# Kernel tuning notes

Measured on AMD Instinct MI355X. Metric: run time of the kernel, lower is better.

Reference implementation:

```python
import jax, jax.numpy as jnp
import numpy as np

B, N, D = 4, 2048, 256
EPS = 1e-5


def _clinear(Z, W, b):
    # complex linear: Z (B,2,N,din), W (2,dout,din), b (2,dout)
    Zr, Zi = Z[:, 0], Z[:, 1]
    Wr, Wi = W[0], W[1]
    outr = Zr @ Wr.T - Zi @ Wi.T + b[0]
    outi = Zr @ Wi.T + Zi @ Wr.T + b[1]
    return jnp.stack([outr, outi], axis=1)


def setup_inputs() -> dict:
    key = jax.random.key(0)
    ks = jax.random.split(key, 14)
    sc = 1.0 / np.sqrt(D).astype(np.float32)
    t = jnp.tile(jnp.arange(N + 1, dtype=jnp.float32)[None] * 0.01, (B, 1))
    return {
        'Z_q': jax.random.normal(ks[0], (B, 2, N, D), jnp.float32),
        'Z_k': jax.random.normal(ks[1], (B, 2, N, D), jnp.float32),
        'Z_v': jax.random.normal(ks[2], (B, 2, N, D), jnp.float32),
        't_measure_all': t,
        'W_q': jax.random.normal(ks[3], (2, D, D), jnp.float32) * sc,
        'b_q': jax.random.normal(ks[4], (2, D), jnp.float32) * 0.01,
        'W_k': jax.random.normal(ks[5], (2, D, D), jnp.float32) * sc,
        'b_k': jax.random.normal(ks[6], (2, D), jnp.float32) * 0.01,
        'W_v': jax.random.normal(ks[7], (2, D, D), jnp.float32) * sc,
        'b_v': jax.random.normal(ks[8], (2, D), jnp.float32) * 0.01,
        'W_p': jax.random.normal(ks[9], (2, D, D), jnp.float32) * sc,
        'b_p': jax.random.normal(ks[10], (2, D), jnp.float32) * 0.01,
        'lambda1': jax.random.normal(ks[11], (2, D // 2, 1), jnp.float32),
        'lambda_Omega_sqrt': jax.random.normal(ks[12], (1, D, 1), jnp.float32) * sc,
        'lambda_Gamma_sqrt': jax.random.normal(ks[13], (1, D, 1), jnp.float32) * sc,
        'tau': jnp.asarray(1.0, jnp.float32),
        'delta': jnp.asarray(0.0, jnp.float32),
        'lambda_C': jnp.ones((1, D, 1), jnp.float32),
    }


def reference(Z_q, Z_k, Z_v, t_measure_all, W_q, b_q, W_k, b_k, W_v, b_v,
              W_p, b_p, lambda1, lambda_Omega_sqrt, lambda_Gamma_sqrt,
              tau, delta, lambda_C):
    # lambda_h = 0 * compute_lambda_h(lambda1): conjugate-pair spectrum, zeroed in forward
    lam_r = 0.0 * jnp.concatenate([lambda1[0], lambda1[0]], axis=0)[:, 0]   # (D,)
    lam_i = 0.0 * jnp.concatenate([lambda1[1], -lambda1[1]], axis=0)[:, 0]  # (D,)
    lam_Om = lambda_Omega_sqrt ** 2 + EPS   # process noise (1,D,1)
    lam_Ga = lambda_Gamma_sqrt ** 2 + EPS   # measurement noise (1,D,1)

    Q = _clinear(Z_q, W_q, b_q)  # (B,2,N,D)
    K = _clinear(Z_k, W_k, b_k)
    V = _clinear(Z_v, W_v, b_v)

    t = t_measure_all[0, :-1]  # (N,)
    # exponential state-transition kernels exp(+/- lambda * t): (2,N,D)
    mag_f = jnp.exp(lam_r[None] * t[:, None]); ph_f = lam_i[None] * t[:, None]
    exp_f = jnp.stack([mag_f * jnp.cos(ph_f), mag_f * jnp.sin(ph_f)])
    mag_b = jnp.exp(-lam_r[None] * t[:, None]); ph_b = -lam_i[None] * t[:, None]
    exp_b = jnp.stack([mag_b * jnp.cos(ph_b), mag_b * jnp.sin(ph_b)])
    # one-step transition exp(lambda * dt): (2,D)
    dt = t[1] - t[0]
    mat_exp = jnp.stack([jnp.exp(lam_r * dt) * jnp.cos(lam_i * dt),
                         jnp.exp(lam_r * dt) * jnp.sin(lam_i * dt)])

    # averaged covariance kernel, exact lambda->0 limit: Gamma + Omega*|t_i-t_j|, mean over D
    lamC2 = lambda_C[0, :, 0] ** 2
    ga_bar = jnp.mean(lamC2 * lam_Ga[0, :, 0])
    om_bar = jnp.mean(lamC2 * lam_Om[0, :, 0])
    abs_dt = jnp.abs(t[:, None] - t[None, :])          # (N,N)
    V_avg_ij = ga_bar + om_bar * abs_dt                # (N,N)

    # factorized kernels
    V_v = exp_f[None]                 # (1,2,N,D)
    U_q = exp_b[None] * Q             # (B,2,N,D)
    U_k = exp_b[None] * K
    U_v = exp_b[None] * V

    # precision-weighted squared residual norm R_ij = sum_d |V_k|^2 |U_q_i - U_k_j|^2
    Vk_abs = jnp.sum(exp_f ** 2, axis=0)              # (N,D)
    Uk_abs = jnp.sum(U_k ** 2, axis=1)                # (B,N,D)
    Uq_abs = jnp.sum(U_q ** 2, axis=1)                # (B,N,D)
    T1 = jnp.einsum('id,bjd->bij', Vk_abs, Uk_abs)
    T2 = jnp.sum(Vk_abs[None] * Uq_abs, axis=2)[:, :, None]
    T3 = (jnp.einsum('bid,bjd->bij', Vk_abs[None] * U_q[:, 0], U_k[:, 0]) +
          jnp.einsum('bid,bjd->bij', Vk_abs[None] * U_q[:, 1], U_k[:, 1]))
    R_qk_abs = T1 + T2 - 2.0 * T3                     # (B,N,N)

    scores = -(tau ** 2) * jnp.log(V_avg_ij[None] + R_qk_abs)
    mask = jnp.tril(jnp.ones((N, N), bool))
    scores = jnp.where(mask[None], scores, -jnp.inf)
    A = jax.nn.softmax(scores, axis=2)                # (B,N,N)
    Q_ij = jnp.stack([A, jnp.zeros_like(A)], axis=1)  # (B,2,N,N)

    # est_inner = complex matmul(Q_ij, U_v); Q imag part is zero
    est_inner = jnp.stack([jnp.einsum('bij,bjd->bid', A, U_v[:, 0]),
                           jnp.einsum('bij,bjd->bid', A, U_v[:, 1])], axis=1)
    est_v = V_v * est_inner          # plain elementwise product, as in source
    s = jax.nn.sigmoid(delta)
    est_eigenbasis = (1.0 - s) * V + s * est_v        # (B,2,N,D)

    # complex Hadamard with one-step transition
    pr = mat_exp[0][None, None] * est_eigenbasis[:, 0] - mat_exp[1][None, None] * est_eigenbasis[:, 1]
    pi = mat_exp[0][None, None] * est_eigenbasis[:, 1] + mat_exp[1][None, None] * est_eigenbasis[:, 0]
    pred_p = jnp.stack([pr, pi], axis=1)
    out = _clinear(pred_p, W_p, b_p)                  # (B,2,N,D)

    lambda_h = jnp.stack([lam_r, lam_i])[..., None]
    return est_eigenbasis, out, Q_ij, V_v, U_v, lambda_h
```

## Files before the change

### kernel.cpp

```cpp
#include <hip/hip_runtime.h>
#include <math.h>

#define BN 4
#define NN 2048
#define DD 256
#define EPSF 1e-5f

typedef __attribute__((ext_vector_type(8))) short bf16x8;
typedef __attribute__((ext_vector_type(4))) float f32x4;

constexpr size_t OFF_EST = 0;
constexpr size_t OFF_OUT = (size_t)BN * 2 * NN * DD;
constexpr size_t OFF_QIJ = OFF_OUT + (size_t)BN * 2 * NN * DD;
constexpr size_t OFF_VV  = OFF_QIJ + (size_t)BN * 2 * NN * NN;
constexpr size_t OFF_UV  = OFF_VV + (size_t)2 * NN * DD;
constexpr size_t OFF_LH  = OFF_UV + (size_t)BN * 2 * NN * DD;

constexpr size_t SCR_B0   = OFF_QIJ + (size_t)NN * NN;
constexpr size_t U_Q16    = 0;
constexpr size_t U_K16    = (size_t)BN * NN * DD;
constexpr size_t U_VT16   = 2 * (size_t)BN * NN * DD;
constexpr size_t SCR_QN   = SCR_B0 + 3 * (size_t)BN * NN * DD / 2;
constexpr size_t SCR_KN   = SCR_QN + (size_t)BN * NN;
constexpr size_t SCR_L    = SCR_KN + (size_t)BN * NN;
constexpr size_t SCR_SC   = SCR_L + (size_t)BN * NN;
constexpr size_t SCR_E16F = OFF_QIJ + 3 * (size_t)NN * NN;
constexpr size_t SCR_Z16F = OFF_QIJ + 5 * (size_t)NN * NN;
constexpr size_t SCR_Z16VF = OFF_QIJ + 7 * (size_t)NN * NN;
constexpr size_t U_W16    = (size_t)BN * NN * 512;

__device__ __forceinline__ short f2bf(float x) {
    union { float f; unsigned u; } v; v.f = x;
    unsigned r = v.u + 0x7fff + ((v.u >> 16) & 1);
    return (short)(r >> 16);
}
__device__ __forceinline__ float bf2f(unsigned short h) {
    union { unsigned u; float f; } v; v.u = ((unsigned)h) << 16;
    return v.f;
}
__device__ __forceinline__ unsigned short* u16p(float* d, size_t fofs) {
    return (unsigned short*)(d + fofs);
}
__device__ __forceinline__ const unsigned short* u16pc(const float* d, size_t fofs) {
    return (const unsigned short*)(d + fofs);
}

__global__ void k_prep(const float* __restrict__ tau, const float* __restrict__ delta,
                       const float* __restrict__ lamOm, const float* __restrict__ lamGa,
                       const float* __restrict__ lamC, float* __restrict__ dout) {
    __shared__ float red[8];
    const int t = threadIdx.x;
    float c2 = lamC[t] * lamC[t];
    float ga = c2 * (lamGa[t] * lamGa[t] + EPSF);
    float om = c2 * (lamOm[t] * lamOm[t] + EPSF);
    for (int o = 32; o > 0; o >>= 1) {
        ga += __shfl_down(ga, o, 64);
        om += __shfl_down(om, o, 64);
    }
    if ((t & 63) == 0) { red[t >> 6] = ga; red[4 + (t >> 6)] = om; }
    __syncthreads();
    if (t == 0) {
        float gs = red[0] + red[1] + red[2] + red[3];
        float os = red[4] + red[5] + red[6] + red[7];
        float* scal = dout + SCR_SC;
        scal[0] = tau[0] * tau[0];
        scal[1] = 1.f / (1.f + __expf(-delta[0]));
        scal[2] = gs / 256.f;
        scal[3] = os / 256.f;
    }
    float* Z = dout + SCR_QN;
    for (int i = t; i < 3 * BN * NN; i += 256) Z[i] = 0.f;
}

__global__ void k_zero_est(float* __restrict__ dout) {
    const int b = blockIdx.y;
    float* p = dout + OFF_EST + (size_t)(2 * b) * NN * DD;
    const size_t i = ((size_t)blockIdx.x * 256 + threadIdx.x) * 4;
    *(float4*)&p[i] = (float4){0.f, 0.f, 0.f, 0.f};
}

__global__ void k_cvt(const float* __restrict__ Zq, const float* __restrict__ Zk,
                      const float* __restrict__ Zv,
                      const float* __restrict__ Wq, const float* __restrict__ Wk,
                      const float* __restrict__ Wv, const float* __restrict__ Wp,
                      float* __restrict__ dout) {
    const int z = blockIdx.z;
    if (z < 3) {
        const float* Z = (z == 0) ? Zq : (z == 1) ? Zk : Zv;
        unsigned short* O = (z == 0) ? u16p(dout, SCR_Z16F)
                          : (z == 1) ? u16p(dout, SCR_Z16F) + (size_t)BN * NN * 512
                                     : u16p(dout, SCR_Z16VF);
        const long n4 = (long)BN * 2 * NN * DD / 4;
        for (long i4 = (long)blockIdx.x * 256 + threadIdx.x; i4 < n4;
             i4 += (long)gridDim.x * 256) {
            const long i = i4 * 4;
            const int d = (int)(i & (DD - 1));
            const long r = i >> 8;
            const int n = (int)(r & (NN - 1));
            const long bc = r >> 11;
            const int c = (int)(bc & 1), b = (int)(bc >> 1);
            float4 v = *(const float4*)&Z[i];
            ushort4 o;
            o.x = (unsigned short)f2bf(v.x); o.y = (unsigned short)f2bf(v.y);
            o.z = (unsigned short)f2bf(v.z); o.w = (unsigned short)f2bf(v.w);
            *(ushort4*)&O[((size_t)(b * NN + n)) * 512 + c * 256 + d] = o;
        }
    } else {
        const float* Ws[4] = {Wq, Wk, Wv, Wp};
        unsigned short* W16 = u16p(dout, SCR_Z16VF) + U_W16;
        const long n4 = 6L * 256 * 512 / 4;
        for (long e4 = (long)blockIdx.x * 256 + threadIdx.x; e4 < n4;
             e4 += (long)gridDim.x * 256) {
            const long e = e4 * 4;
            const int k = (int)(e & 511);
            const long rest = e >> 9;
            const int dd = (int)(rest & 255);
            const int m = (int)(rest >> 8);
            int proj, mode;
            if (m < 3)      { proj = m; mode = 0; }
            else if (m == 3){ proj = 2; mode = 1; }
            else            { proj = 3; mode = m - 4; }
            const int kc = k >> 8, kk = k & 255;
            int wc; float sgn;
            if (mode == 0) { wc = kc; sgn = kc ? -1.f : 1.f; }
            else           { wc = 1 - kc; sgn = 1.f; }
            float4 v = *(const float4*)&Ws[proj][((size_t)wc * DD + dd) * DD + kk];
            ushort4 o;
            o.x = (unsigned short)f2bf(sgn * v.x); o.y = (unsigned short)f2bf(sgn * v.y);
            o.z = (unsigned short)f2bf(sgn * v.z); o.w = (unsigned short)f2bf(sgn * v.w);
            *(ushort4*)&W16[(size_t)m * 256 * 512 + (size_t)dd * 512 + k] = o;
        }
    }
}

__global__ __launch_bounds__(256) void k_qkv(const float* __restrict__ bq,
                                             const float* __restrict__ bk,
                                             const float* __restrict__ bv,
                                             float* __restrict__ dout)
{
    __shared__ short Al[128 * 40];
    __shared__ short Bl[128 * 40];
    const int z = blockIdx.z;
    const int d0 = blockIdx.x * 128;
    const int b = blockIdx.y >> 4;
    const int n0 = (blockIdx.y & 15) * 128;

    const unsigned short* Z16 =
        (z == 0) ? u16pc(dout, SCR_Z16F)
      : (z == 1) ? u16pc(dout, SCR_Z16F) + (size_t)BN * NN * 512
                 : u16pc(dout, SCR_Z16VF);
    const unsigned short* W16 = u16pc(dout, SCR_Z16VF) + U_W16 + (size_t)z * 256 * 512;
    const float* bias = (z == 0) ? bq : (z == 1) ? bk : bv;
    const int bofs = (z == 3) ? DD : 0;

    const int t = threadIdx.x, wave = t >> 6, lane = t & 63, quad = lane >> 4, lm = lane & 15;
    const int wm = (wave >> 1) * 64, wn = (wave & 1) * 64;
    const int srow = t >> 1, sch = (t & 1) * 16;

    f32x4 acc[4][4];
#pragma unroll
    for (int i = 0; i < 4; ++i)
#pragma unroll
        for (int j = 0; j < 4; ++j) acc[i][j] = (f32x4){0.f, 0.f, 0.f, 0.f};

    for (int kt = 0; kt < 16; ++kt) {
        const int kk0 = kt * 32;
        const unsigned short* Za = Z16 + ((size_t)(b * NN + n0 + srow)) * 512 + kk0 + sch;
        bf16x8 a0 = *(const bf16x8*)(Za + 0);
        bf16x8 a1 = *(const bf16x8*)(Za + 8);
        const unsigned short* Wa = W16 + (size_t)(d0 + srow) * 512 + kk0 + sch;
        bf16x8 w0 = *(const bf16x8*)(Wa + 0);
        bf16x8 w1 = *(const bf16x8*)(Wa + 8);
        __syncthreads();
        *(bf16x8*)&Al[srow * 40 + sch]     = a0;
        *(bf16x8*)&Al[srow * 40 + sch + 8] = a1;
        *(bf16x8*)&Bl[srow * 40 + sch]     = w0;
        *(bf16x8*)&Bl[srow * 40 + sch + 8] = w1;
        __syncthreads();
        bf16x8 af[4], bff[4];
#pragma unroll
        for (int mi = 0; mi < 4; ++mi) af[mi] = *(const bf16x8*)&Al[(wm + mi * 16 + lm) * 40 + quad * 8];
#pragma unroll
        for (int nj = 0; nj < 4; ++nj) bff[nj] = *(const bf16x8*)&Bl[(wn + nj * 16 + lm) * 40 + quad * 8];
#pragma unroll
        for (int mi = 0; mi < 4; ++mi)
#pragma unroll
            for (int nj = 0; nj < 4; ++nj)
                acc[mi][nj] = __builtin_amdgcn_mfma_f32_16x16x32_bf16(af[mi], bff[nj], acc[mi][nj], 0, 0, 0);
    }

    if (z <= 1) {
        unsigned short* O16 = u16p(dout, SCR_B0) + (z ? U_K16 : U_Q16) + (size_t)b * NN * DD;
        float* NRM = dout + (z ? SCR_KN : SCR_QN) + b * NN;
#pragma unroll
        for (int mi = 0; mi < 4; ++mi)
#pragma unroll
            for (int r = 0; r < 4; ++r) {
                const int m = n0 + wm + mi * 16 + quad * 4 + r;
                float ss = 0.f;
#pragma unroll
                for (int nj = 0; nj < 4; ++nj) {
                    const int d = d0 + wn + nj * 16 + lm;
                    unsigned short h = (unsigned short)f2bf(acc[mi][nj][r] + bias[d]);
                    O16[(size_t)m * DD + d] = h;
                    const float vb = bf2f(h);
                    ss = fmaf(vb, vb, ss);
                }
                ss += __shfl_down(ss, 8, 16); ss += __shfl_down(ss, 4, 16);
                ss += __shfl_down(ss, 2, 16); ss += __shfl_down(ss, 1, 16);
                if (lm == 0) atomicAdd(&NRM[m], ss);
            }
    } else if (z == 2) {
        float* UV0 = dout + OFF_UV + (size_t)(b * 2) * NN * DD;
#pragma unroll
        for (int mi = 0; mi < 4; ++mi)
#pragma unroll
            for (int r = 0; r < 4; ++r) {
                const int m = n0 + wm + mi * 16 + quad * 4 + r;
#pragma unroll
                for (int nj = 0; nj < 4; ++nj) {
                    const int d = d0 + wn + nj * 16 + lm;
                    UV0[(size_t)m * DD + d] = acc[mi][nj][r] + bias[d];
                }
            }
    } else {
        const float s1 = 1.f - dout[SCR_SC + 1];
        float* EST1 = dout + OFF_EST + (size_t)(b * 2 + 1) * NN * DD;
        unsigned short* E16 = u16p(dout, SCR_E16F) + (size_t)b * NN * 512;
#pragma unroll
        for (int mi = 0; mi < 4; ++mi)
#pragma unroll
            for (int r = 0; r < 4; ++r) {
                const int m = n0 + wm + mi * 16 + quad * 4 + r;
#pragma unroll
                for (int nj = 0; nj < 4; ++nj) {
                    const int d = d0 + wn + nj * 16 + lm;
                    const float v = s1 * (acc[mi][nj][r] + bias[bofs + d]);
                    EST1[(size_t)m * DD + d] = v;
                    E16[(size_t)m * 512 + 256 + d] = (unsigned short)f2bf(v);
                }
            }
    }
}

__global__ __launch_bounds__(256) void k_outproj(const float* __restrict__ bp,
                                                 float* __restrict__ dout)
{
    __shared__ short Al[128 * 40];
    __shared__ short Bl[128 * 40];
    const int z = blockIdx.z;
    const int d0 = blockIdx.x * 128;
    const int b = blockIdx.y >> 4;
    const int n0 = (blockIdx.y & 15) * 128;
    const unsigned short* E16 = u16pc(dout, SCR_E16F) + (size_t)b * NN * 512;
    const unsigned short* W16 = u16pc(dout, SCR_Z16VF) + U_W16 + (size_t)(4 + z) * 256 * 512;

    const int t = threadIdx.x, wave = t >> 6, lane = t & 63, quad = lane >> 4, lm = lane & 15;
    const int wm = (wave >> 1) * 64, wn = (wave & 1) * 64;
    const int srow = t >> 1, sch = (t & 1) * 16;

    f32x4 acc[4][4];
#pragma unroll
    for (int i = 0; i < 4; ++i)
#pragma unroll
        for (int j = 0; j < 4; ++j) acc[i][j] = (f32x4){0.f, 0.f, 0.f, 0.f};

    for (int kt = 0; kt < 16; ++kt) {
        const int kk0 = kt * 32;
        const unsigned short* Za = E16 + ((size_t)(n0 + srow)) * 512 + kk0 + sch;
        bf16x8 a0 = *(const bf16x8*)(Za + 0);
        bf16x8 a1 = *(const bf16x8*)(Za + 8);
        const unsigned short* Wa = W16 + (size_t)(d0 + srow) * 512 + kk0 + sch;
        bf16x8 w0 = *(const bf16x8*)(Wa + 0);
        bf16x8 w1 = *(const bf16x8*)(Wa + 8);
        __syncthreads();
        *(bf16x8*)&Al[srow * 40 + sch]     = a0;
        *(bf16x8*)&Al[srow * 40 + sch + 8] = a1;
        *(bf16x8*)&Bl[srow * 40 + sch]     = w0;
        *(bf16x8*)&Bl[srow * 40 + sch + 8] = w1;
        __syncthreads();
        bf16x8 af[4], bff[4];
#pragma unroll
        for (int mi = 0; mi < 4; ++mi) af[mi] = *(const bf16x8*)&Al[(wm + mi * 16 + lm) * 40 + quad * 8];
#pragma unroll
        for (int nj = 0; nj < 4; ++nj) bff[nj] = *(const bf16x8*)&Bl[(wn + nj * 16 + lm) * 40 + quad * 8];
#pragma unroll
        for (int mi = 0; mi < 4; ++mi)
#pragma unroll
            for (int nj = 0; nj < 4; ++nj)
                acc[mi][nj] = __builtin_amdgcn_mfma_f32_16x16x32_bf16(af[mi], bff[nj], acc[mi][nj], 0, 0, 0);
    }
    const int bofs = z ? DD : 0;
    float* O = dout + OFF_OUT + (size_t)(b * 2 + z) * NN * DD;
#pragma unroll
    for (int mi = 0; mi < 4; ++mi)
#pragma unroll
        for (int r = 0; r < 4; ++r) {
            const int m = n0 + wm + mi * 16 + quad * 4 + r;
#pragma unroll
            for (int nj = 0; nj < 4; ++nj) {
                const int d = d0 + wn + nj * 16 + lm;
                O[(size_t)m * DD + d] = acc[mi][nj][r] + bp[bofs + d];
            }
        }
}

__global__ void k_vtrans(float* __restrict__ dout) {
    __shared__ float T[64][65];
    const int b = blockIdx.z;
    const int nb = blockIdx.x * 64, db = blockIdx.y * 64;
    const float* V = dout + OFF_UV + (size_t)(b * 2) * NN * DD;
    unsigned short* VT = u16p(dout, SCR_B0) + U_VT16 + (size_t)b * DD * NN;
    const int tr = threadIdx.x >> 4, tc = (threadIdx.x & 15) * 4;
#pragma unroll
    for (int p = 0; p < 4; ++p) {
        float4 v = *(const float4*)&V[(size_t)(nb + tr + p * 16) * DD + db + tc];
        T[tr + p * 16][tc + 0] = v.x; T[tr + p * 16][tc + 1] = v.y;
        T[tr + p * 16][tc + 2] = v.z; T[tr + p * 16][tc + 3] = v.w;
    }
    __syncthreads();
#pragma unroll
    for (int p = 0; p < 4; ++p) {
        const int d = tr + p * 16;
        ushort4 o;
        o.x = (unsigned short)f2bf(T[tc + 0][d]);
        o.y = (unsigned short)f2bf(T[tc + 1][d]);
        o.z = (unsigned short)f2bf(T[tc + 2][d]);
        o.w = (unsigned short)f2bf(T[tc + 3][d]);
        *(ushort4*)&VT[(size_t)(db + d) * NN + nb + tc] = o;
    }
}

__global__ __launch_bounds__(256) void k_scores(const float* __restrict__ tmeas,
                                                float* __restrict__ dout) {
    __shared__ short Al[128 * 40];
    __shared__ short Bl[128 * 40];
    const int b = blockIdx.y, x = blockIdx.x;
    int ti = (int)((sqrtf(8.f * x + 1.f) - 1.f) * 0.5f);
    while ((ti + 1) * (ti + 2) / 2 <= x) ++ti;
    while (ti * (ti + 1) / 2 > x) --ti;
    const int tj = x - ti * (ti + 1) / 2;
    const int i0 = ti * 128, j0 = tj * 128;
    const unsigned short* Q16 = u16pc(dout, SCR_B0) + U_Q16 + (size_t)b * NN * DD;
    const unsigned short* K16 = u16pc(dout, SCR_B0) + U_K16 + (size_t)b * NN * DD;
    const int t = threadIdx.x, wave = t >> 6, lane = t & 63, quad = lane >> 4, lm = lane & 15;
    const int wm = (wave >> 1) * 64, wn = (wave & 1) * 64;
    const int srow = t >> 1, sch = (t & 1) * 16;

    f32x4 acc[4][4];
#pragma unroll
    for (int i = 0; i < 4; ++i)
#pragma unroll
        for (int j = 0; j < 4; ++j) acc[i][j] = (f32x4){0.f, 0.f, 0.f, 0.f};

    for (int kt = 0; kt < 8; ++kt) {
        const int kk0 = kt * 32;
        bf16x8 q0 = *(const bf16x8*)(Q16 + (size_t)(i0 + srow) * DD + kk0 + sch);
        bf16x8 q1 = *(const bf16x8*)(Q16 + (size_t)(i0 + srow) * DD + kk0 + sch + 8);
        bf16x8 k0 = *(const bf16x8*)(K16 + (size_t)(j0 + srow) * DD + kk0 + sch);
        bf16x8 k1 = *(const bf16x8*)(K16 + (size_t)(j0 + srow) * DD + kk0 + sch + 8);
        __syncthreads();
        *(bf16x8*)&Al[srow * 40 + sch]     = q0;
        *(bf16x8*)&Al[srow * 40 + sch + 8] = q1;
        *(bf16x8*)&Bl[srow * 40 + sch]     = k0;
        *(bf16x8*)&Bl[srow * 40 + sch + 8] = k1;
        __syncthreads();
        bf16x8 af[4], bff[4];
#pragma unroll
        for (int mi = 0; mi < 4; ++mi) af[mi] = *(const bf16x8*)&Al[(wm + mi * 16 + lm) * 40 + quad * 8];
#pragma unroll
        for (int nj = 0; nj < 4; ++nj) bff[nj] = *(const bf16x8*)&Bl[(wn + nj * 16 + lm) * 40 + quad * 8];
#pragma unroll
        for (int mi = 0; mi < 4; ++mi)
#pragma unroll
            for (int nj = 0; nj < 4; ++nj)
                acc[mi][nj] = __builtin_amdgcn_mfma_f32_16x16x32_bf16(af[mi], bff[nj], acc[mi][nj], 0, 0, 0);
    }

    const float tau2 = dout[SCR_SC + 0], ga = dout[SCR_SC + 2], om = dout[SCR_SC + 3];
    float* Qij = dout + OFF_QIJ + (size_t)b * 2 * NN * NN;
    const float* QN_ = dout + SCR_QN + b * NN;
    const float* KN_ = dout + SCR_KN + b * NN;
    float kn[4], tjv[4]; int jj[4];
#pragma unroll
    for (int nj = 0; nj < 4; ++nj) {
        jj[nj] = j0 + wn + nj * 16 + lm;
        kn[nj] = KN_[jj[nj]];
        tjv[nj] = tmeas[jj[nj]];
    }
#pragma unroll
    for (int mi = 0; mi < 4; ++mi)
#pragma unroll
        for (int r = 0; r < 4; ++r) {
            const int i = i0 + wm + mi * 16 + quad * 4 + r;
            const float qni = QN_[i], tqi = tmeas[i];
            float rs = 0.f;
#pragma unroll
            for (int nj = 0; nj < 4; ++nj) {
                float xx = ga + om * fabsf(tqi - tjv[nj]) + qni + kn[nj] - 2.f * acc[mi][nj][r];
                xx = fmaxf(xx, 1e-30f);
                float w = (tau2 == 1.f) ? (1.f / xx) : __expf(-tau2 * __logf(xx));
                if (jj[nj] > i) w = 0.f;
                Qij[(size_t)i * NN + jj[nj]] = w;
                rs += w;
            }
            rs += __shfl_down(rs, 8, 16); rs += __shfl_down(rs, 4, 16);
            rs += __shfl_down(rs, 2, 16); rs += __shfl_down(rs, 1, 16);
            if (lm == 0) atomicAdd(&dout[SCR_L + b * NN + i], rs);
        }
}

__global__ __launch_bounds__(512) void k_estinner(float* __restrict__ dout) {
    __shared__ short Al[128 * 40];
    __shared__ short Bl[256 * 40];
    const int b = blockIdx.y;
    int y = blockIdx.x, TI = 0;
    for (;;) { const int nc = (TI + 2) >> 1; if (y < nc) break; y -= nc; ++TI; }
    const int i0 = TI * 128;
    const int kbeg = y * 256;
    const int kend = min(kbeg + 256, (TI + 1) * 128);
    const int nst = (kend - kbeg) >> 5;
    float* Qij = dout + OFF_QIJ + (size_t)b * 2 * NN * NN;
    const unsigned short* VT = u16pc(dout, SCR_B0) + U_VT16 + (size_t)b * DD * NN;

    const int t = threadIdx.x, wave = t >> 6, lane = t & 63, quad = lane >> 4, lm = lane & 15;
    const int wm = (wave >> 2) * 64, wn = (wave & 3) * 64;
    const int arow = t >> 2, acol = (t & 3) * 8;
    const int vrow = t >> 1, vcol = (t & 1) * 16;
    const float linv = 1.f / dout[SCR_L + b * NN + i0 + arow];

    f32x4 acc[4][4];
#pragma unroll
    for (int i = 0; i < 4; ++i)
#pragma unroll
        for (int j = 0; j < 4; ++j) acc[i][j] = (f32x4){0.f, 0.f, 0.f, 0.f};

    for (int kt = 0; kt < nst; ++kt) {
        const int kk0 = kbeg + kt * 32;
        float* Ap = &Qij[(size_t)(i0 + arow) * NN + kk0 + acol];
        float4 w0 = *(const float4*)(Ap + 0);
        float4 w1 = *(const float4*)(Ap + 4);
        w0.x *= linv; w0.y *= linv; w0.z *= linv; w0.w *= linv;
        w1.x *= linv; w1.y *= linv; w1.z *= linv; w1.w *= linv;
        bf16x8 pa;
        pa[0] = f2bf(w0.x); pa[1] = f2bf(w0.y); pa[2] = f2bf(w0.z); pa[3] = f2bf(w0.w);
        pa[4] = f2bf(w1.x); pa[5] = f2bf(w1.y); pa[6] = f2bf(w1.z); pa[7] = f2bf(w1.w);
        bf16x8 v0 = *(const bf16x8*)(VT + (size_t)vrow * NN + kk0 + vcol);
        bf16x8 v1 = *(const bf16x8*)(VT + (size_t)vrow * NN + kk0 + vcol + 8);
        *(float4*)(Ap + 0) = w0;
        *(float4*)(Ap + 4) = w1;
        __syncthreads();
        *(bf16x8*)&Al[arow * 40 + acol] = pa;
        *(bf16x8*)&Bl[vrow * 40 + vcol]     = v0;
        *(bf16x8*)&Bl[vrow * 40 + vcol + 8] = v1;
        __syncthreads();
        bf16x8 af[4], bff[4];
#pragma unroll
        for (int mi = 0; mi < 4; ++mi) af[mi] = *(const bf16x8*)&Al[(wm + mi * 16 + lm) * 40 + quad * 8];
#pragma unroll
        for (int nj = 0; nj < 4; ++nj) bff[nj] = *(const bf16x8*)&Bl[(wn + nj * 16 + lm) * 40 + quad * 8];
#pragma unroll
        for (int mi = 0; mi < 4; ++mi)
#pragma unroll
            for (int nj = 0; nj < 4; ++nj)
                acc[mi][nj] = __builtin_amdgcn_mfma_f32_16x16x32_bf16(af[mi], bff[nj], acc[mi][nj], 0, 0, 0);
    }
    float* EST = dout + OFF_EST + (size_t)(b * 2) * NN * DD;
#pragma unroll
    for (int mi = 0; mi < 4; ++mi)
#pragma unroll
        for (int r = 0; r < 4; ++r) {
            const int i = i0 + wm + mi * 16 + quad * 4 + r;
#pragma unroll
            for (int nj = 0; nj < 4; ++nj) {
                const int d = wn + nj * 16 + lm;
                atomicAdd(&EST[(size_t)i * DD + d], acc[mi][nj][r]);
            }
        }
}

__global__ void k_blend(float* __restrict__ dout) {
    const int b = blockIdx.y, i = blockIdx.x;
    const float s = dout[SCR_SC + 1];
    float* e = dout + OFF_EST + ((size_t)(b * 2) * NN + i) * DD + threadIdx.x * 4;
    const float* vr = dout + OFF_UV + ((size_t)(b * 2) * NN + i) * DD + threadIdx.x * 4;
    unsigned short* E16 = u16p(dout, SCR_E16F) + ((size_t)(b * NN + i)) * 512 + threadIdx.x * 4;
    float4 ev = *(float4*)e;
    float4 vv = *(const float4*)vr;
    ev.x = (1.f - s) * vv.x + s * ev.x;
    ev.y = (1.f - s) * vv.y + s * ev.y;
    ev.z = (1.f - s) * vv.z + s * ev.z;
    ev.w = (1.f - s) * vv.w + s * ev.w;
    *(float4*)e = ev;
    ushort4 o;
    o.x = (unsigned short)f2bf(ev.x); o.y = (unsigned short)f2bf(ev.y);
    o.z = (unsigned short)f2bf(ev.z); o.w = (unsigned short)f2bf(ev.w);
    *(ushort4*)E16 = o;
}

__global__ void k_fills(float* __restrict__ dout) {
    const int z = blockIdx.z;
    if (z >= 11) {
        const int b = z - 11, i = blockIdx.x;
        const int jstart = ((i >> 7) + 1) << 7;
        float* row = dout + OFF_QIJ + (size_t)b * 2 * NN * NN + (size_t)i * NN;
        const float4 zz = {0.f, 0.f, 0.f, 0.f};
        for (int j = jstart + threadIdx.x * 4; j < NN; j += 256 * 4)
            *(float4*)&row[j] = zz;
        return;
    }
    size_t base; long n; float val = 0.f;
    if (z < 4)       { base = OFF_QIJ + (size_t)(2 * z + 1) * NN * NN; n = (long)NN * NN; }
    else if (z == 4) { base = OFF_VV; n = (long)NN * DD; val = 1.f; }
    else if (z == 5) { base = OFF_VV + (size_t)NN * DD; n = (long)NN * DD; }
    else if (z < 10) { base = OFF_UV + (size_t)(2 * (z - 6) + 1) * NN * DD; n = (long)NN * DD; }
    else             { base = OFF_LH; n = 512; }
    float* p = dout + base;
    const float4 v = {val, val, val, val};
    for (long i = ((long)blockIdx.x * 256 + threadIdx.x) * 4; i < n;
         i += (long)gridDim.x * 1024)
        *(float4*)&p[i] = v;
}

extern "C" void kernel_launch(void* const* d_in, const int* in_sizes, int n_in,
                              void* d_out, int out_size, void* d_ws, size_t ws_size,
                              hipStream_t stream) {
    const float* Zq = (const float*)d_in[0];
    const float* Zk = (const float*)d_in[1];
    const float* Zv = (const float*)d_in[2];
    const float* tm = (const float*)d_in[3];
    const float* Wq = (const float*)d_in[4];
    const float* bq = (const float*)d_in[5];
    const float* Wk = (const float*)d_in[6];
    const float* bk = (const float*)d_in[7];
    const float* Wv = (const float*)d_in[8];
    const float* bv = (const float*)d_in[9];
    const float* Wp = (const float*)d_in[10];
    const float* bp = (const float*)d_in[11];
    const float* lamOm = (const float*)d_in[13];
    const float* lamGa = (const float*)d_in[14];
    const float* tau = (const float*)d_in[15];
    const float* delta = (const float*)d_in[16];
    const float* lamC = (const float*)d_in[17];
    float* out = (float*)d_out;

    k_prep<<<dim3(1), dim3(256), 0, stream>>>(tau, delta, lamOm, lamGa, lamC, out);
    k_cvt<<<dim3(2048, 1, 4), dim3(256), 0, stream>>>(Zq, Zk, Zv, Wq, Wk, Wv, Wp, out);
    k_zero_est<<<dim3(512, 4), dim3(256), 0, stream>>>(out);
    k_qkv<<<dim3(2, 64, 4), dim3(256), 0, stream>>>(bq, bk, bv, out);
    k_vtrans<<<dim3(32, 4, 4), dim3(256), 0, stream>>>(out);
    k_scores<<<dim3(136, 4), dim3(256), 0, stream>>>(tm, out);
    k_estinner<<<dim3(72, 4), dim3(512), 0, stream>>>(out);
    k_blend<<<dim3(2048, 4), dim3(64), 0, stream>>>(out);
    k_outproj<<<dim3(2, 64, 2), dim3(256), 0, stream>>>(bp, out);
    k_fills<<<dim3(2048, 1, 15), dim3(256), 0, stream>>>(out);
}
```

Measured before the change: 368.9 us.

## Replace atomic est_inner accumulation with bf16 split-K partials reduced in fused blend/fill

The est_inner kernel now splits the causal K range into chunks of up to 768 columns (30 blocks per batch instead of 72) and writes bf16 partial tiles to scratch rather than doing fp32 atomicAdds into the output. A combined blend+fills kernel sums the partials, applies the sigmoid blend, and writes both fp32 and bf16 estimates, while also zero-filling the scratch regions of Q_ij. The prep and zero-est kernels are folded into the conversion launch, which cuts the launch count. The bf16 partials lose precision, fewer est_inner blocks lower parallelism, and an extra tail kernel is added to clear the scratch used by the outproj.

Result: faster. 354.6 us (-3.9%).

```diff
diff --git a/kernel.cpp b/kernel.cpp
--- a/kernel.cpp
+++ b/kernel.cpp
@@ -24,7 +24,9 @@
 constexpr size_t SCR_KN   = SCR_QN + (size_t)BN * NN;
 constexpr size_t SCR_L    = SCR_KN + (size_t)BN * NN;
 constexpr size_t SCR_SC   = SCR_L + (size_t)BN * NN;
+constexpr size_t SCR_W16P = SCR_SC + 16;
 constexpr size_t SCR_E16F = OFF_QIJ + 3 * (size_t)NN * NN;
+constexpr size_t U_PART   = (size_t)BN * NN * 512;
 constexpr size_t SCR_Z16F = OFF_QIJ + 5 * (size_t)NN * NN;
 constexpr size_t SCR_Z16VF = OFF_QIJ + 7 * (size_t)NN * NN;
 constexpr size_t U_W16    = (size_t)BN * NN * 512;
@@ -44,45 +46,18 @@
 __device__ __forceinline__ const unsigned short* u16pc(const float* d, size_t fofs) {
     return (const unsigned short*)(d + fofs);
 }
-
-__global__ void k_prep(const float* __restrict__ tau, const float* __restrict__ delta,
-                       const float* __restrict__ lamOm, const float* __restrict__ lamGa,
-                       const float* __restrict__ lamC, float* __restrict__ dout) {
-    __shared__ float red[8];
-    const int t = threadIdx.x;
-    float c2 = lamC[t] * lamC[t];
-    float ga = c2 * (lamGa[t] * lamGa[t] + EPSF);
-    float om = c2 * (lamOm[t] * lamOm[t] + EPSF);
-    for (int o = 32; o > 0; o >>= 1) {
-        ga += __shfl_down(ga, o, 64);
-        om += __shfl_down(om, o, 64);
-    }
-    if ((t & 63) == 0) { red[t >> 6] = ga; red[4 + (t >> 6)] = om; }
-    __syncthreads();
-    if (t == 0) {
-        float gs = red[0] + red[1] + red[2] + red[3];
-        float os = red[4] + red[5] + red[6] + red[7];
-        float* scal = dout + SCR_SC;
-        scal[0] = tau[0] * tau[0];
-        scal[1] = 1.f / (1.f + __expf(-delta[0]));
-        scal[2] = gs / 256.f;
-        scal[3] = os / 256.f;
-    }
-    float* Z = dout + SCR_QN;
-    for (int i = t; i < 3 * BN * NN; i += 256) Z[i] = 0.f;
-}
-
-__global__ void k_zero_est(float* __restrict__ dout) {
-    const int b = blockIdx.y;
-    float* p = dout + OFF_EST + (size_t)(2 * b) * NN * DD;
-    const size_t i = ((size_t)blockIdx.x * 256 + threadIdx.x) * 4;
-    *(float4*)&p[i] = (float4){0.f, 0.f, 0.f, 0.f};
+__device__ __forceinline__ int nc_of(int TI) { return TI >= 12 ? 3 : (TI >= 6 ? 2 : 1); }
+__device__ __forceinline__ int cb_of(int TI) {
+    return TI < 6 ? TI : (TI < 12 ? 6 + 2 * (TI - 6) : 18 + 3 * (TI - 12));
 }
 
 __global__ void k_cvt(const float* __restrict__ Zq, const float* __restrict__ Zk,
                       const float* __restrict__ Zv,
                       const float* __restrict__ Wq, const float* __restrict__ Wk,
                       const float* __restrict__ Wv, const float* __restrict__ Wp,
+                      const float* __restrict__ tau, const float* __restrict__ delta,
+                      const float* __restrict__ lamOm, const float* __restrict__ lamGa,
+                      const float* __restrict__ lamC,
                       float* __restrict__ dout) {
     const int z = blockIdx.z;
     if (z < 3) {
@@ -105,9 +80,8 @@
             o.z = (unsigned short)f2bf(v.z); o.w = (unsigned short)f2bf(v.w);
             *(ushort4*)&O[((size_t)(b * NN + n)) * 512 + c * 256 + d] = o;
         }
-    } else {
+    } else if (z == 3) {
         const float* Ws[4] = {Wq, Wk, Wv, Wp};
-        unsigned short* W16 = u16p(dout, SCR_Z16VF) + U_W16;
         const long n4 = 6L * 256 * 512 / 4;
         for (long e4 = (long)blockIdx.x * 256 + threadIdx.x; e4 < n4;
              e4 += (long)gridDim.x * 256) {
@@ -128,7 +102,35 @@
             ushort4 o;
             o.x = (unsigned short)f2bf(sgn * v.x); o.y = (unsigned short)f2bf(sgn * v.y);
             o.z = (unsigned short)f2bf(sgn * v.z); o.w = (unsigned short)f2bf(sgn * v.w);
-            *(ushort4*)&W16[(size_t)m * 256 * 512 + (size_t)dd * 512 + k] = o;
+            unsigned short* dst = (m < 4)
+                ? u16p(dout, SCR_Z16VF) + U_W16 + (size_t)m * 131072
+                : u16p(dout, SCR_W16P) + (size_t)(m - 4) * 131072;
+            *(ushort4*)&dst[(size_t)dd * 512 + k] = o;
+        }
+    } else {
+        const int idx = blockIdx.x * 256 + threadIdx.x;
+        if (idx < 3 * BN * NN) dout[SCR_QN + idx] = 0.f;
+        if (blockIdx.x == 0) {
+            __shared__ float red[8];
+            const int t = threadIdx.x;
+            float c2 = lamC[t] * lamC[t];
+            float ga = c2 * (lamGa[t] * lamGa[t] + EPSF);
+            float om = c2 * (lamOm[t] * lamOm[t] + EPSF);
+            for (int o = 32; o > 0; o >>= 1) {
+                ga += __shfl_down(ga, o, 64);
+                om += __shfl_down(om, o, 64);
+            }
+            if ((t & 63) == 0) { red[t >> 6] = ga; red[4 + (t >> 6)] = om; }
+            __syncthreads();
+            if (t == 0) {
+                float gs = red[0] + red[1] + red[2] + red[3];
+                float os = red[4] + red[5] + red[6] + red[7];
+                float* scal = dout + SCR_SC;
+                scal[0] = tau[0] * tau[0];
+                scal[1] = 1.f / (1.f + __expf(-delta[0]));
+                scal[2] = gs / 256.f;
+                scal[3] = os / 256.f;
+            }
         }
     }
 }
@@ -149,7 +151,7 @@
         (z == 0) ? u16pc(dout, SCR_Z16F)
       : (z == 1) ? u16pc(dout, SCR_Z16F) + (size_t)BN * NN * 512
                  : u16pc(dout, SCR_Z16VF);
-    const unsigned short* W16 = u16pc(dout, SCR_Z16VF) + U_W16 + (size_t)z * 256 * 512;
+    const unsigned short* W16 = u16pc(dout, SCR_Z16VF) + U_W16 + (size_t)z * 131072;
     const float* bias = (z == 0) ? bq : (z == 1) ? bk : bv;
     const int bofs = (z == 3) ? DD : 0;
 
@@ -253,7 +255,7 @@
     const int b = blockIdx.y >> 4;
     const int n0 = (blockIdx.y & 15) * 128;
     const unsigned short* E16 = u16pc(dout, SCR_E16F) + (size_t)b * NN * 512;
-    const unsigned short* W16 = u16pc(dout, SCR_Z16VF) + U_W16 + (size_t)(4 + z) * 256 * 512;
+    const unsigned short* W16 = u16pc(dout, SCR_W16P) + (size_t)z * 131072;
 
     const int t = threadIdx.x, wave = t >> 6, lane = t & 63, quad = lane >> 4, lm = lane & 15;
     const int wm = (wave >> 1) * 64, wn = (wave & 1) * 64;
@@ -414,12 +416,13 @@
     __shared__ short Al[128 * 40];
     __shared__ short Bl[256 * 40];
     const int b = blockIdx.y;
-    int y = blockIdx.x, TI = 0;
-    for (;;) { const int nc = (TI + 2) >> 1; if (y < nc) break; y -= nc; ++TI; }
+    int y = blockIdx.x, TI = 0, cb = 0;
+    for (;;) { const int nc = nc_of(TI); if (y < nc) break; y -= nc; cb += nc; ++TI; }
     const int i0 = TI * 128;
-    const int kbeg = y * 256;
-    const int kend = min(kbeg + 256, (TI + 1) * 128);
+    const int kbeg = y * 768;
+    const int kend = min(kbeg + 768, (TI + 1) * 128);
     const int nst = (kend - kbeg) >> 5;
+    const int cidx = cb + y;
     float* Qij = dout + OFF_QIJ + (size_t)b * 2 * NN * NN;
     const unsigned short* VT = u16pc(dout, SCR_B0) + U_VT16 + (size_t)b * DD * NN;
 
@@ -465,43 +468,54 @@
             for (int nj = 0; nj < 4; ++nj)
                 acc[mi][nj] = __builtin_amdgcn_mfma_f32_16x16x32_bf16(af[mi], bff[nj], acc[mi][nj], 0, 0, 0);
     }
-    float* EST = dout + OFF_EST + (size_t)(b * 2) * NN * DD;
+    unsigned short* P = u16p(dout, SCR_E16F) + U_PART +
+                        ((size_t)(b * 30 + cidx)) * 128 * 256;
 #pragma unroll
     for (int mi = 0; mi < 4; ++mi)
 #pragma unroll
         for (int r = 0; r < 4; ++r) {
-            const int i = i0 + wm + mi * 16 + quad * 4 + r;
+            const int ri = wm + mi * 16 + quad * 4 + r;
 #pragma unroll
             for (int nj = 0; nj < 4; ++nj) {
                 const int d = wn + nj * 16 + lm;
-                atomicAdd(&EST[(size_t)i * DD + d], acc[mi][nj][r]);
-            }
-        }
-}
-
-__global__ void k_blend(float* __restrict__ dout) {
-    const int b = blockIdx.y, i = blockIdx.x;
-    const float s = dout[SCR_SC + 1];
-    float* e = dout + OFF_EST + ((size_t)(b * 2) * NN + i) * DD + threadIdx.x * 4;
-    const float* vr = dout + OFF_UV + ((size_t)(b * 2) * NN + i) * DD + threadIdx.x * 4;
-    unsigned short* E16 = u16p(dout, SCR_E16F) + ((size_t)(b * NN + i)) * 512 + threadIdx.x * 4;
-    float4 ev = *(float4*)e;
-    float4 vv = *(const float4*)vr;
-    ev.x = (1.f - s) * vv.x + s * ev.x;
-    ev.y = (1.f - s) * vv.y + s * ev.y;
-    ev.z = (1.f - s) * vv.z + s * ev.z;
-    ev.w = (1.f - s) * vv.w + s * ev.w;
-    *(float4*)e = ev;
-    ushort4 o;
-    o.x = (unsigned short)f2bf(ev.x); o.y = (unsigned short)f2bf(ev.y);
-    o.z = (unsigned short)f2bf(ev.z); o.w = (unsigned short)f2bf(ev.w);
-    *(ushort4*)E16 = o;
-}
-
-__global__ void k_fills(float* __restrict__ dout) {
+                P[(size_t)ri * 256 + d] = (unsigned short)f2bf(acc[mi][nj][r]);
+            }
+        }
+}
+
+__global__ void k_blendfills(float* __restrict__ dout) {
     const int z = blockIdx.z;
-    if (z >= 11) {
-        const int b = z - 11, i = blockIdx.x;
+    if (z < 4) {
+        const int b = z;
+        if (blockIdx.x >= 512) return;
+        const int t = threadIdx.x;
+        const int i = blockIdx.x * 4 + (t >> 6);
+        const int d4 = (t & 63) * 4;
+        const int TI = i >> 7;
+        const int nc = nc_of(TI), cb = cb_of(TI);
+        const float s = dout[SCR_SC + 1];
+        const unsigned short* P = u16pc(dout, SCR_E16F) + U_PART;
+        float4 sum = {0.f, 0.f, 0.f, 0.f};
+        for (int c = 0; c < nc; ++c) {
+            ushort4 pv = *(const ushort4*)&P[((size_t)(b * 30 + cb + c) * 128 + (i & 127)) * 256 + d4];
+            sum.x += bf2f(pv.x); sum.y += bf2f(pv.y);
+            sum.z += bf2f(pv.z); sum.w += bf2f(pv.w);
+        }
+        const float4 vr = *(const float4*)&dout[OFF_UV + ((size_t)(b * 2) * NN + i) * DD + d4];
+        float4 ev;
+        ev.x = (1.f - s) * vr.x + s * sum.x;
+        ev.y = (1.f - s) * vr.y + s * sum.y;
+        ev.z = (1.f - s) * vr.z + s * sum.z;
+        ev.w = (1.f - s) * vr.w + s * sum.w;
+        *(float4*)&dout[OFF_EST + ((size_t)(b * 2) * NN + i) * DD + d4] = ev;
+        ushort4 o;
+        o.x = (unsigned short)f2bf(ev.x); o.y = (unsigned short)f2bf(ev.y);
+        o.z = (unsigned short)f2bf(ev.z); o.w = (unsigned short)f2bf(ev.w);
+        *(ushort4*)&u16p(dout, SCR_E16F)[((size_t)(b * NN + i)) * 512 + d4] = o;
+        return;
+    }
+    if (z < 8) {
+        const int b = z - 4, i = blockIdx.x;
         const int jstart = ((i >> 7) + 1) << 7;
         float* row = dout + OFF_QIJ + (size_t)b * 2 * NN * NN + (size_t)i * NN;
         const float4 zz = {0.f, 0.f, 0.f, 0.f};
@@ -510,16 +524,30 @@
         return;
     }
     size_t base; long n; float val = 0.f;
-    if (z < 4)       { base = OFF_QIJ + (size_t)(2 * z + 1) * NN * NN; n = (long)NN * NN; }
-    else if (z == 4) { base = OFF_VV; n = (long)NN * DD; val = 1.f; }
-    else if (z == 5) { base = OFF_VV + (size_t)NN * DD; n = (long)NN * DD; }
-    else if (z < 10) { base = OFF_UV + (size_t)(2 * (z - 6) + 1) * NN * DD; n = (long)NN * DD; }
-    else             { base = OFF_LH; n = 512; }
+    if (z == 8)       { base = SCR_B0; n = 3145728; }
+    else if (z == 9)  { base = SCR_Z16F; n = (long)NN * NN; }
+    else if (z == 10) { base = SCR_Z16VF; n = (long)NN * NN; }
+    else if (z == 11) { base = OFF_VV; n = (long)NN * DD; val = 1.f; }
+    else if (z == 12) { base = OFF_VV + (size_t)NN * DD; n = (long)NN * DD; }
+    else if (z < 17)  { base = OFF_UV + (size_t)(2 * (z - 13) + 1) * NN * DD; n = (long)NN * DD; }
+    else              { base = OFF_LH; n = 512; }
     float* p = dout + base;
     const float4 v = {val, val, val, val};
     for (long i = ((long)blockIdx.x * 256 + threadIdx.x) * 4; i < n;
          i += (long)gridDim.x * 1024)
         *(float4*)&p[i] = v;
+}
+
+__global__ void k_tail(float* __restrict__ dout) {
+    const float4 zz = {0.f, 0.f, 0.f, 0.f};
+    const long n1 = (long)NN * NN;
+    for (long i = ((long)blockIdx.x * 256 + threadIdx.x) * 4; i < n1;
+         i += (long)gridDim.x * 1024)
+        *(float4*)&dout[SCR_E16F + i] = zz;
+    const long n0 = (long)NN * NN - 3145728;
+    for (long i = ((long)blockIdx.x * 256 + threadIdx.x) * 4; i < n0;
+         i += (long)gridDim.x * 1024)
+        *(float4*)&dout[SCR_QN + i] = zz;
 }
 
 extern "C" void kernel_launch(void* const* d_in, const int* in_sizes, int n_in,
@@ -544,14 +572,13 @@
     const float* lamC = (const float*)d_in[17];
     float* out = (float*)d_out;
 
-    k_prep<<<dim3(1), dim3(256), 0, stream>>>(tau, delta, lamOm, lamGa, lamC, out);
-    k_cvt<<<dim3(2048, 1, 4), dim3(256), 0, stream>>>(Zq, Zk, Zv, Wq, Wk, Wv, Wp, out);
-    k_zero_est<<<dim3(512, 4), dim3(256), 0, stream>>>(out);
+    k_cvt<<<dim3(2048, 1, 5), dim3(256), 0, stream>>>(
+        Zq, Zk, Zv, Wq, Wk, Wv, Wp, tau, delta, lamOm, lamGa, lamC, out);
     k_qkv<<<dim3(2, 64, 4), dim3(256), 0, stream>>>(bq, bk, bv, out);
     k_vtrans<<<dim3(32, 4, 4), dim3(256), 0, stream>>>(out);
     k_scores<<<dim3(136, 4), dim3(256), 0, stream>>>(tm, out);
-    k_estinner<<<dim3(72, 4), dim3(512), 0, stream>>>(out);
-    k_blend<<<dim3(2048, 4), dim3(64), 0, stream>>>(out);
+    k_estinner<<<dim3(30, 4), dim3(512), 0, stream>>>(out);
+    k_blendfills<<<dim3(2048, 1, 18), dim3(256), 0, stream>>>(out);
     k_outproj<<<dim3(2, 64, 2), dim3(256), 0, stream>>>(bp, out);
-    k_fills<<<dim3(2048, 1, 15), dim3(256), 0, stream>>>(out);
-}
+    k_tail<<<dim3(2048), dim3(256), 0, stream>>>(out);
+}
```
